# Optimization experiments

Hardware: AMD Instinct MI355X
Metric: run time of the kernel (lower is better)

The kernel has to match this reference:

```python
import jax, jax.numpy as jnp
import numpy as np

NEG_SLOPE = 0.01  # torch LeakyReLU default
BN_EPS = 1e-5

def leaky_relu(x):
    return jnp.where(x >= 0, x, NEG_SLOPE * x)

def setup_inputs() -> dict:
    key = jax.random.key(0)
    kx, kw, k1w, k1b, k2w, k2b = jax.random.split(key, 6)
    B, S, d = 512, 256, 64
    H, E = 64, 8  # n_hidden_sets, n_elements
    X = jax.random.normal(kx, (B, S, d), dtype=jnp.float32)
    # Wc ~ U(-1, 1) per init_weights
    Wc = jax.random.uniform(kw, (d, H * E), dtype=jnp.float32, minval=-1.0, maxval=1.0)
    # Linear layers: torch default init ~ U(-1/sqrt(fan_in), 1/sqrt(fan_in))
    b1 = 1.0 / np.sqrt(H)
    fc1_w = jax.random.uniform(k1w, (32, H), dtype=jnp.float32, minval=-b1, maxval=b1)
    fc1_b = jax.random.uniform(k1b, (32,), dtype=jnp.float32, minval=-b1, maxval=b1)
    b2 = 1.0 / np.sqrt(32)
    fc2_w = jax.random.uniform(k2w, (1, 32), dtype=jnp.float32, minval=-b2, maxval=b2)
    fc2_b = jax.random.uniform(jax.random.fold_in(key, 7), (1,), dtype=jnp.float32, minval=-b2, maxval=b2)
    gamma = jnp.ones((32,), dtype=jnp.float32)
    beta = jnp.zeros((32,), dtype=jnp.float32)
    return {"X": X, "Wc": Wc, "fc1_w": fc1_w, "fc1_b": fc1_b,
            "gamma": gamma, "beta": beta, "fc2_w": fc2_w, "fc2_b": fc2_b}

def reference(X, Wc, fc1_w, fc1_b, gamma, beta, fc2_w, fc2_b):
    B, S, d = X.shape
    HE = Wc.shape[1]
    H = fc1_w.shape[1]          # n_hidden_sets
    E = HE // H                 # n_elements
    # [B,S,d] @ [d,H*E] -> [B,S,H*E], LeakyReLU epilogue
    t = leaky_relu(jnp.matmul(X, Wc))
    # torch .view: row-major reshape to [B,S,E,H]
    t = t.reshape(B, S, E, H)
    t = jnp.max(t, axis=2)      # max over elements -> [B,S,H]
    t = jnp.sum(t, axis=1)      # sum over set -> [B,H]
    # fc1
    t = t @ fc1_w.T + fc1_b     # [B,32]
    # BatchNorm1d, training-mode batch statistics (biased var)
    mu = jnp.mean(t, axis=0)
    var = jnp.mean(jnp.square(t - mu), axis=0)
    t = (t - mu) * jax.lax.rsqrt(var + BN_EPS) * gamma + beta
    t = leaky_relu(t)
    out = t @ fc2_w.T + fc2_b   # [B,1]
    return out[:, 0]
```

## Files before the change

kernel.cpp:

```cpp
#include <hip/hip_runtime.h>

typedef __bf16 bf16x4 __attribute__((ext_vector_type(4)));
typedef __bf16 bf16x8 __attribute__((ext_vector_type(8)));
typedef float  f32x4  __attribute__((ext_vector_type(4)));

#define WCS 68
#define XS  68

__global__ __launch_bounds__(256, 2)
void fused_main(const float* __restrict__ X, const float* __restrict__ Wc,
                const float* __restrict__ fc1_w, const float* __restrict__ fc1_b,
                float* __restrict__ out1)
{
    __shared__ __bf16 wclds[512 * WCS];
    __shared__ __bf16 xlds[64 * XS];
    __shared__ float  t0row[64];

    const int tid  = threadIdx.x;
    const int b    = blockIdx.x;
    const int wave = tid >> 6;
    const int lane = tid & 63;
    const int n    = lane & 15;
    const int q    = lane >> 4;

    #pragma unroll
    for (int cc = 0; cc < 2; ++cc) {
        const int c = tid + cc * 256;
        #pragma unroll
        for (int kc = 0; kc < 8; ++kc) {
            bf16x4 lo, hi;
            #pragma unroll
            for (int j = 0; j < 4; ++j) lo[j] = (__bf16)Wc[(kc * 8 + j) * 512 + c];
            #pragma unroll
            for (int j = 0; j < 4; ++j) hi[j] = (__bf16)Wc[(kc * 8 + 4 + j) * 512 + c];
            *(bf16x4*)&wclds[c * WCS + kc * 8]     = lo;
            *(bf16x4*)&wclds[c * WCS + kc * 8 + 4] = hi;
        }
    }

    float hsum = 0.0f;

    for (int st = 0; st < 4; ++st) {
        const float4* xg = (const float4*)(X + ((size_t)b * 256 + (size_t)st * 64) * 64);
        #pragma unroll
        for (int i = 0; i < 4; ++i) {
            const int p = tid + i * 256;
            float4 v = xg[p];
            bf16x4 o;
            o[0] = (__bf16)v.x; o[1] = (__bf16)v.y;
            o[2] = (__bf16)v.z; o[3] = (__bf16)v.w;
            const int r = p >> 4, ck = p & 15;
            *(bf16x4*)&xlds[r * XS + ck * 4] = o;
        }
        __syncthreads();

        bf16x8 a0[4], a1[4];
        #pragma unroll
        for (int t = 0; t < 4; ++t) {
            const int base = (t * 16 + n) * XS + q * 8;
            bf16x4 p0 = *(const bf16x4*)&xlds[base];
            bf16x4 p1 = *(const bf16x4*)&xlds[base + 4];
            bf16x4 p2 = *(const bf16x4*)&xlds[base + 32];
            bf16x4 p3 = *(const bf16x4*)&xlds[base + 36];
            a0[t] = __builtin_shufflevector(p0, p1, 0, 1, 2, 3, 4, 5, 6, 7);
            a1[t] = __builtin_shufflevector(p2, p3, 0, 1, 2, 3, 4, 5, 6, 7);
        }

        float rmax[4][4];
        #pragma unroll
        for (int t = 0; t < 4; ++t)
            #pragma unroll
            for (int r4 = 0; r4 < 4; ++r4) rmax[t][r4] = -3.0e38f;

        for (int e = 0; e < 8; ++e) {
            const int c    = e * 64 + wave * 16 + n;
            const int base = c * WCS + q * 8;
            bf16x4 p0 = *(const bf16x4*)&wclds[base];
            bf16x4 p1 = *(const bf16x4*)&wclds[base + 4];
            bf16x4 p2 = *(const bf16x4*)&wclds[base + 32];
            bf16x4 p3 = *(const bf16x4*)&wclds[base + 36];
            bf16x8 b0 = __builtin_shufflevector(p0, p1, 0, 1, 2, 3, 4, 5, 6, 7);
            bf16x8 b1 = __builtin_shufflevector(p2, p3, 0, 1, 2, 3, 4, 5, 6, 7);
            #pragma unroll
            for (int t = 0; t < 4; ++t) {
                f32x4 acc = {0.f, 0.f, 0.f, 0.f};
                acc = __builtin_amdgcn_mfma_f32_16x16x32_bf16(a0[t], b0, acc, 0, 0, 0);
                acc = __builtin_amdgcn_mfma_f32_16x16x32_bf16(a1[t], b1, acc, 0, 0, 0);
                #pragma unroll
                for (int r4 = 0; r4 < 4; ++r4) {
                    float v = acc[r4];
                    v = fmaxf(v, 0.01f * v);
                    rmax[t][r4] = fmaxf(rmax[t][r4], v);
                }
            }
        }

        float s = 0.f;
        #pragma unroll
        for (int t = 0; t < 4; ++t)
            #pragma unroll
            for (int r4 = 0; r4 < 4; ++r4) s += rmax[t][r4];
        s += __shfl_xor(s, 16);
        s += __shfl_xor(s, 32);
        hsum += s;
        __syncthreads();
    }

    if (lane < 16) t0row[wave * 16 + lane] = hsum;
    __syncthreads();

    if (wave == 0) {
        const int j = lane & 31, half = lane >> 5;
        float p = 0.f;
        #pragma unroll
        for (int i = 0; i < 32; ++i)
            p += t0row[half * 32 + i] * fc1_w[j * 64 + half * 32 + i];
        p += __shfl_xor(p, 32);
        if (half == 0) out1[b * 32 + j] = p + fc1_b[j];
    }
}

__global__ __launch_bounds__(512)
void bn_fc2(const float* __restrict__ out1, const float* __restrict__ gamma,
            const float* __restrict__ beta, const float* __restrict__ fc2_w,
            const float* __restrict__ fc2_b, float* __restrict__ out)
{
    __shared__ float psum[16][32];
    __shared__ float psumsq[16][32];
    __shared__ float sa[32], sc[32];

    const int tid = threadIdx.x;
    const int j   = tid & 31;
    const int sl  = tid >> 5;

    float s = 0.f, ss = 0.f;
    #pragma unroll
    for (int i = 0; i < 32; ++i) {
        float v = out1[(sl * 32 + i) * 32 + j];
        s  += v;
        ss += v * v;
    }
    psum[sl][j]   = s;
    psumsq[sl][j] = ss;
    __syncthreads();

    if (tid < 32) {
        float S = 0.f, SS = 0.f;
        #pragma unroll
        for (int i = 0; i < 16; ++i) { S += psum[i][tid]; SS += psumsq[i][tid]; }
        const float mu  = S * (1.0f / 512.0f);
        const float var = SS * (1.0f / 512.0f) - mu * mu;
        const float rs  = rsqrtf(var + 1e-5f);
        const float a   = rs * gamma[tid];
        sa[tid] = a;
        sc[tid] = beta[tid] - mu * a;
    }
    __syncthreads();

    float acc = 0.f;
    #pragma unroll
    for (int jj = 0; jj < 32; ++jj) {
        float v = out1[tid * 32 + jj];
        float y = v * sa[jj] + sc[jj];
        y = fmaxf(y, 0.01f * y);
        acc += y * fc2_w[jj];
    }
    out[tid] = acc + fc2_b[0];
}

extern "C" void kernel_launch(void* const* d_in, const int* in_sizes, int n_in,
                              void* d_out, int out_size, void* d_ws, size_t ws_size,
                              hipStream_t stream) {
    const float* X      = (const float*)d_in[0];
    const float* Wc     = (const float*)d_in[1];
    const float* fc1_w  = (const float*)d_in[2];
    const float* fc1_b  = (const float*)d_in[3];
    const float* gamma  = (const float*)d_in[4];
    const float* beta   = (const float*)d_in[5];
    const float* fc2_w  = (const float*)d_in[6];
    const float* fc2_b  = (const float*)d_in[7];

    float* out1 = (float*)d_ws;

    fused_main<<<512, 256, 0, stream>>>(X, Wc, fc1_w, fc1_b, out1);
    bn_fc2<<<1, 512, 0, stream>>>(out1, gamma, beta, fc2_w, fc2_b, (float*)d_out);
}
```

Baseline: 99.30 us.

## Keep Wc fragments in registers and prefetch next X tile

```diff
diff --git a/kernel.cpp b/kernel.cpp
--- a/kernel.cpp
+++ b/kernel.cpp
@@ -4,15 +4,13 @@
 typedef __bf16 bf16x8 __attribute__((ext_vector_type(8)));
 typedef float  f32x4  __attribute__((ext_vector_type(4)));
 
-#define WCS 68
-#define XS  68
+#define XS 68
 
 __global__ __launch_bounds__(256, 2)
 void fused_main(const float* __restrict__ X, const float* __restrict__ Wc,
                 const float* __restrict__ fc1_w, const float* __restrict__ fc1_b,
                 float* __restrict__ out1)
 {
-    __shared__ __bf16 wclds[512 * WCS];
     __shared__ __bf16 xlds[64 * XS];
     __shared__ float  t0row[64];
 
@@ -23,36 +21,45 @@
     const int n    = lane & 15;
     const int q    = lane >> 4;
 
+    const float4* xg = (const float4*)(X + (size_t)b * 256 * 64);
+
+    float4 xv[4];
     #pragma unroll
-    for (int cc = 0; cc < 2; ++cc) {
-        const int c = tid + cc * 256;
+    for (int i = 0; i < 4; ++i) xv[i] = xg[tid + i * 256];
+
+    bf16x8 bf0[8], bf1[8];
+    {
+        const float* wbase = Wc + (q * 8) * 512 + wave * 16 + n;
         #pragma unroll
-        for (int kc = 0; kc < 8; ++kc) {
-            bf16x4 lo, hi;
+        for (int e = 0; e < 8; ++e) {
+            const float* p = wbase + e * 64;
             #pragma unroll
-            for (int j = 0; j < 4; ++j) lo[j] = (__bf16)Wc[(kc * 8 + j) * 512 + c];
-            #pragma unroll
-            for (int j = 0; j < 4; ++j) hi[j] = (__bf16)Wc[(kc * 8 + 4 + j) * 512 + c];
-            *(bf16x4*)&wclds[c * WCS + kc * 8]     = lo;
-            *(bf16x4*)&wclds[c * WCS + kc * 8 + 4] = hi;
+            for (int j = 0; j < 8; ++j) {
+                bf0[e][j] = (__bf16)p[j * 512];
+                bf1[e][j] = (__bf16)p[(j + 32) * 512];
+            }
         }
     }
 
     float hsum = 0.0f;
 
     for (int st = 0; st < 4; ++st) {
-        const float4* xg = (const float4*)(X + ((size_t)b * 256 + (size_t)st * 64) * 64);
         #pragma unroll
         for (int i = 0; i < 4; ++i) {
             const int p = tid + i * 256;
-            float4 v = xg[p];
             bf16x4 o;
-            o[0] = (__bf16)v.x; o[1] = (__bf16)v.y;
-            o[2] = (__bf16)v.z; o[3] = (__bf16)v.w;
+            o[0] = (__bf16)xv[i].x; o[1] = (__bf16)xv[i].y;
+            o[2] = (__bf16)xv[i].z; o[3] = (__bf16)xv[i].w;
             const int r = p >> 4, ck = p & 15;
             *(bf16x4*)&xlds[r * XS + ck * 4] = o;
         }
         __syncthreads();
+
+        if (st < 3) {
+            const float4* xgn = xg + (st + 1) * 1024;
+            #pragma unroll
+            for (int i = 0; i < 4; ++i) xv[i] = xgn[tid + i * 256];
+        }
 
         bf16x8 a0[4], a1[4];
         #pragma unroll
@@ -72,25 +79,16 @@
             #pragma unroll
             for (int r4 = 0; r4 < 4; ++r4) rmax[t][r4] = -3.0e38f;
 
+        #pragma unroll
         for (int e = 0; e < 8; ++e) {
-            const int c    = e * 64 + wave * 16 + n;
-            const int base = c * WCS + q * 8;
-            bf16x4 p0 = *(const bf16x4*)&wclds[base];
-            bf16x4 p1 = *(const bf16x4*)&wclds[base + 4];
-            bf16x4 p2 = *(const bf16x4*)&wclds[base + 32];
-            bf16x4 p3 = *(const bf16x4*)&wclds[base + 36];
-            bf16x8 b0 = __builtin_shufflevector(p0, p1, 0, 1, 2, 3, 4, 5, 6, 7);
-            bf16x8 b1 = __builtin_shufflevector(p2, p3, 0, 1, 2, 3, 4, 5, 6, 7);
             #pragma unroll
             for (int t = 0; t < 4; ++t) {
                 f32x4 acc = {0.f, 0.f, 0.f, 0.f};
-                acc = __builtin_amdgcn_mfma_f32_16x16x32_bf16(a0[t], b0, acc, 0, 0, 0);
-                acc = __builtin_amdgcn_mfma_f32_16x16x32_bf16(a1[t], b1, acc, 0, 0, 0);
+                acc = __builtin_amdgcn_mfma_f32_16x16x32_bf16(a0[t], bf0[e], acc, 0, 0, 0);
+                acc = __builtin_amdgcn_mfma_f32_16x16x32_bf16(a1[t], bf1[e], acc, 0, 0, 0);
                 #pragma unroll
                 for (int r4 = 0; r4 < 4; ++r4) {
-                    float v = acc[r4];
-                    v = fmaxf(v, 0.01f * v);
-                    rmax[t][r4] = fmaxf(rmax[t][r4], v);
+                    rmax[t][r4] = fmaxf(rmax[t][r4], fmaxf(acc[r4], 0.01f * acc[r4]));
                 }
             }
         }
```

After: 99.27 us. No clear change (-0.0%).
